# Performance work log

Measured on AMD Instinct MI355X. Metric: run time of the kernel, lower is better.

The kernel has to match this reference:

```python
import jax, jax.numpy as jnp
import numpy as np

N, E, F_IN, H, HEADS, L, DEPTH = 10000, 160000, 128, 64, 8, 6, 3
M = HEADS * H  # 512, fractal transform width
OUT_DIM = 64
EPS = 1e-5
CHAOS = 0.1


def _ln(x, g, b):
    mu = x.mean(-1, keepdims=True)
    var = x.var(-1, keepdims=True)
    return (x - mu) / jnp.sqrt(var + EPS) * g + b


def _ln_plain(x):
    mu = x.mean(-1, keepdims=True)
    var = x.var(-1, keepdims=True)
    return (x - mu) / jnp.sqrt(var + EPS)


def setup_inputs() -> dict:
    key = jax.random.key(0)
    ks = iter(jax.random.split(key, 64))
    r = lambda *s: jax.random.normal(next(ks), s, jnp.float32) * 0.05
    return dict(
        x=jax.random.normal(next(ks), (N, F_IN), jnp.float32),
        edge_index=jax.random.randint(next(ks), (2, E), 0, N),
        enc_W=r(F_IN, H), enc_b=jnp.zeros((H,)), enc_g=jnp.ones((H,)), enc_beta=jnp.zeros((H,)),
        chaos_memory=r(1, H),
        tW0=r(L, H, M), tb0=jnp.zeros((L, M)), tg0=jnp.ones((L, M)), tbeta0=jnp.zeros((L, M)),
        tW1=r(L, M, M), tb1=jnp.zeros((L, M)), tg1=jnp.ones((L, M)), tbeta1=jnp.zeros((L, M)),
        tW2=r(L, M, M), tb2=jnp.zeros((L, M)), tg2=jnp.ones((L, M)), tbeta2=jnp.zeros((L, M)),
        att=r(L, HEADS, 2 * H),
        evo_W1=r(H, 2 * H), evo_b1=jnp.zeros((2 * H,)),
        evo_W2=r(2 * H, H), evo_b2=jnp.zeros((H,)),
        dec_state_W=r(H, 1), dec_state_b=jnp.zeros((1,)),
        dec_imp_W=r(H, 1), dec_imp_b=jnp.zeros((1,)),
        dec_chaos_W=r(H, 1), dec_chaos_b=jnp.zeros((1,)),
        dec_evo_W=r(H, OUT_DIM), dec_evo_b=jnp.zeros((OUT_DIM,)),
    )


def reference(x, edge_index, enc_W, enc_b, enc_g, enc_beta, chaos_memory,
              tW0, tb0, tg0, tbeta0, tW1, tb1, tg1, tbeta1, tW2, tb2, tg2, tbeta2,
              att, evo_W1, evo_b1, evo_W2, evo_b2,
              dec_state_W, dec_state_b, dec_imp_W, dec_imp_b,
              dec_chaos_W, dec_chaos_b, dec_evo_W, dec_evo_b):
    src, dst = edge_index[0], edge_index[1]  # j -> i, aggregate at dst
    nkey = jax.random.key(42)

    # encoder (dropout inactive in eval)
    h = jax.nn.relu(_ln(x @ enc_W + enc_b, enc_g, enc_beta))
    h = h + chaos_memory * CHAOS  # [1,H] broadcast

    residuals = []
    for i in range(L):
        cf = CHAOS * (1.0 + 0.1 * i)
        h_prev = h
        # fractal transform stack: pre-noise features are averaged
        Ws = [(tW0[i], tb0[i], tg0[i], tbeta0[i]),
              (tW1[i], tb1[i], tg1[i], tbeta1[i]),
              (tW2[i], tb2[i], tg2[i], tbeta2[i])]
        cur = h
        feats = 0.0
        for d, (W, b, g, be) in enumerate(Ws):
            cur = jax.nn.relu(_ln(cur @ W + b, g, be))
            feats = feats + cur
            noise = jax.random.normal(jax.random.fold_in(nkey, i * 10 + d), cur.shape, cur.dtype)
            cur = cur + noise * cf  # chaotic perturbation feeds next depth only
        hm = (feats / DEPTH).reshape(-1, HEADS, H)  # [N, heads, out]
        # GAT-style edge attention: alpha_e = <[x_i||x_j], att>
        a_i = jnp.einsum('nhc,hc->nh', hm, att[i][:, :H])
        a_j = jnp.einsum('nhc,hc->nh', hm, att[i][:, H:])
        alpha = jax.nn.leaky_relu(a_i[dst] + a_j[src], 0.2)  # [E, heads]
        # segment softmax over incoming edges of each dst node
        amax = jax.ops.segment_max(alpha, dst, num_segments=N)
        ex = jnp.exp(alpha - amax[dst])
        denom = jax.ops.segment_sum(ex, dst, num_segments=N)
        w = ex / denom[dst]  # [E, heads]
        msg = hm[src] * w[:, :, None]  # [E, heads, out]
        agg = jax.ops.segment_sum(msg, dst, num_segments=N)  # [N, heads, out]
        h_new = agg.mean(axis=1)  # head-mean -> [N, H]
        gate = jax.nn.sigmoid(jnp.tanh(jax.nn.relu(h_new @ evo_W1 + evo_b1) @ evo_W2 + evo_b2))
        h = gate * h_new + (1.0 - gate) * h_prev
        residuals.append(h)
        h = _ln_plain(h)  # F.layer_norm without affine
    h_multi = sum(residuals) / L
    # batch is None -> decoders applied per-node on h_multi
    state = h_multi @ dec_state_W + dec_state_b
    importance = h_multi @ dec_imp_W + dec_imp_b
    chaos = h_multi @ dec_chaos_W + dec_chaos_b
    evolution = h_multi @ dec_evo_W + dec_evo_b
    return state, importance, chaos, evolution, h_multi
```

## Files before the change

### kernel.cpp

```cpp
#include <hip/hip_runtime.h>
#include <cstdint>
#include <cstddef>

#define NN 10000
#define EE 160000
#define F_IN 128
#define HH 64
#define HEADS 8
#define LL 6
#define MM 512
#define OUT_DIM 64
#define EPSF 1e-5f

typedef unsigned short ushort;
typedef __attribute__((ext_vector_type(8))) short bf16x8;
typedef __attribute__((ext_vector_type(8))) unsigned short ushort8;
typedef __attribute__((ext_vector_type(4))) float f32x4;

union U8 { ushort8 u; bf16x8 b; };

struct U2 { uint32_t a, b; };

__host__ __device__ constexpr uint32_t rotl32(uint32_t x, uint32_t d) {
  return (x << d) | (x >> (32u - d));
}

__host__ __device__ constexpr U2 threefry2x32(uint32_t k1, uint32_t k2, uint32_t x0, uint32_t x1) {
  uint32_t ks2 = k1 ^ k2 ^ 0x1BD11BDAu;
  x0 += k1; x1 += k2;
  x0 += x1; x1 = rotl32(x1, 13); x1 ^= x0;
  x0 += x1; x1 = rotl32(x1, 15); x1 ^= x0;
  x0 += x1; x1 = rotl32(x1, 26); x1 ^= x0;
  x0 += x1; x1 = rotl32(x1, 6);  x1 ^= x0;
  x0 += k2; x1 += ks2 + 1u;
  x0 += x1; x1 = rotl32(x1, 17); x1 ^= x0;
  x0 += x1; x1 = rotl32(x1, 29); x1 ^= x0;
  x0 += x1; x1 = rotl32(x1, 16); x1 ^= x0;
  x0 += x1; x1 = rotl32(x1, 24); x1 ^= x0;
  x0 += ks2; x1 += k1 + 2u;
  x0 += x1; x1 = rotl32(x1, 13); x1 ^= x0;
  x0 += x1; x1 = rotl32(x1, 15); x1 ^= x0;
  x0 += x1; x1 = rotl32(x1, 26); x1 ^= x0;
  x0 += x1; x1 = rotl32(x1, 6);  x1 ^= x0;
  x0 += k1; x1 += k2 + 3u;
  x0 += x1; x1 = rotl32(x1, 17); x1 ^= x0;
  x0 += x1; x1 = rotl32(x1, 29); x1 ^= x0;
  x0 += x1; x1 = rotl32(x1, 16); x1 ^= x0;
  x0 += x1; x1 = rotl32(x1, 24); x1 ^= x0;
  x0 += k2; x1 += ks2 + 4u;
  x0 += x1; x1 = rotl32(x1, 13); x1 ^= x0;
  x0 += x1; x1 = rotl32(x1, 15); x1 ^= x0;
  x0 += x1; x1 = rotl32(x1, 26); x1 ^= x0;
  x0 += x1; x1 = rotl32(x1, 6);  x1 ^= x0;
  x0 += ks2; x1 += k1 + 5u;
  return U2{x0, x1};
}

__host__ __device__ constexpr U2 foldKey(uint32_t data) {
  return threefry2x32(0u, 42u, 0u, data);
}

__device__ inline float erfinv_f32(float x) {
  float w = -log1pf(-x * x);
  float p;
  if (w < 5.0f) {
    w -= 2.5f;
    p = 2.81022636e-08f;
    p = fmaf(p, w, 3.43273939e-07f);
    p = fmaf(p, w, -3.5233877e-06f);
    p = fmaf(p, w, -4.39150654e-06f);
    p = fmaf(p, w, 0.00021858087f);
    p = fmaf(p, w, -0.00125372503f);
    p = fmaf(p, w, -0.00417768164f);
    p = fmaf(p, w, 0.246640727f);
    p = fmaf(p, w, 1.50140941f);
  } else {
    w = sqrtf(w) - 3.0f;
    p = -0.000200214257f;
    p = fmaf(p, w, 0.000100950558f);
    p = fmaf(p, w, 0.00134934322f);
    p = fmaf(p, w, -0.00367342844f);
    p = fmaf(p, w, 0.00573950773f);
    p = fmaf(p, w, -0.0076224613f);
    p = fmaf(p, w, 0.00943887047f);
    p = fmaf(p, w, 1.00167406f);
    p = fmaf(p, w, 2.83297682f);
  }
  return p * x;
}

__device__ inline float jax_normal(uint32_t k1, uint32_t k2, uint32_t idx) {
  U2 r = threefry2x32(k1, k2, 0u, idx);
  uint32_t bits = r.a ^ r.b;
  uint32_t fb = (bits >> 9) | 0x3f800000u;
  float f = __uint_as_float(fb) - 1.0f;
  const float lo = -0.99999994f;
  float u = f * 2.0f + lo;
  u = fmaxf(lo, u);
  return 1.41421356f * erfinv_f32(u);
}

__device__ inline float waveSum(float v) {
  v += __shfl_xor(v, 32, 64);
  v += __shfl_xor(v, 16, 64);
  v += __shfl_xor(v, 8, 64);
  v += __shfl_xor(v, 4, 64);
  v += __shfl_xor(v, 2, 64);
  v += __shfl_xor(v, 1, 64);
  return v;
}

__device__ inline ushort bf16rn(float x) {
  uint32_t u = __float_as_uint(x);
  uint32_t r = (u + 0x7fffu + ((u >> 16) & 1u)) >> 16;
  return (ushort)r;
}
__device__ inline float bf16tof(ushort h) {
  return __uint_as_float(((uint32_t)h) << 16);
}


__global__ __launch_bounds__(64) void encoder_kernel(
    const float* __restrict__ x, const float* __restrict__ W, const float* __restrict__ b,
    const float* __restrict__ g, const float* __restrict__ be, const float* __restrict__ cm,
    float* __restrict__ h, ushort* __restrict__ hHi, ushort* __restrict__ hLo) {
  __shared__ float xs[F_IN];
  int n = blockIdx.x, l = threadIdx.x;
  xs[l]      = x[(size_t)n * F_IN + l];
  xs[l + 64] = x[(size_t)n * F_IN + 64 + l];
  __syncthreads();
  float acc = b[l];
  #pragma unroll 8
  for (int k = 0; k < F_IN; k++) acc = fmaf(xs[k], W[k * HH + l], acc);
  float mu = waveSum(acc) * (1.0f / 64.0f);
  float d = acc - mu;
  float var = waveSum(d * d) * (1.0f / 64.0f);
  float y = fmaf(d / sqrtf(var + EPSF), g[l], be[l]);
  y = fmaxf(y, 0.0f);
  float hv = fmaf(cm[l], 0.1f, y);
  h[(size_t)n * HH + l] = hv;
  ushort hi = bf16rn(hv);
  size_t oi = ((size_t)(l >> 5) * NN + n) * 32 + (l & 31);
  hHi[oi] = hi;
  hLo[oi] = bf16rn(hv - bf16tof(hi));
}

__global__ __launch_bounds__(256) void wconv(
    const float* __restrict__ W, ushort* __restrict__ oh, ushort* __restrict__ ol, int K) {
  __shared__ ushort Th[64][40], Tl[64][40];
  int kt = blockIdx.x;
  int m0 = blockIdx.y * 64;
  int lay = blockIdx.z;
  const float* Wl = W + (size_t)lay * K * MM;
  ushort* ohl = oh + (size_t)lay * K * MM;
  ushort* oll = ol + (size_t)lay * K * MM;
  int t = threadIdx.x;
  #pragma unroll
  for (int p = 0; p < 2; ++p) {
    int li = p * 256 + t;
    int k = li >> 4, mg = (li & 15) * 4;
    float4 v = *(const float4*)(Wl + (size_t)(kt * 32 + k) * MM + m0 + mg);
    float vv[4] = {v.x, v.y, v.z, v.w};
    #pragma unroll
    for (int q = 0; q < 4; ++q) {
      ushort hi = bf16rn(vv[q]);
      Th[mg + q][k] = hi;
      Tl[mg + q][k] = bf16rn(vv[q] - bf16tof(hi));
    }
  }
  __syncthreads();
  #pragma unroll
  for (int p = 0; p < 2; ++p) {
    int li = p * 256 + t;
    int plane = li >> 8;
    int rem = li & 255;
    int m = rem >> 2, kh = (rem & 3) * 8;
    size_t go = ((size_t)kt * MM + m0 + m) * 32 + kh;
    if (plane == 0) *(ushort8*)(ohl + go) = *(const ushort8*)&Th[m][kh];
    else            *(ushort8*)(oll + go) = *(const ushort8*)&Tl[m][kh];
  }
}

__global__ __launch_bounds__(256) void gemm_mfma(
    const ushort* __restrict__ Ahg, const ushort* __restrict__ Alg,
    const ushort* __restrict__ Whg, const ushort* __restrict__ Wlg,
    const float* __restrict__ bias, float* __restrict__ C, int nkt) {
  __shared__ __align__(16) ushort Ah[128][36], Al[128][36];
  __shared__ __align__(16) ushort Bh[64][36],  Bl[64][36];
  int t = threadIdx.x, w = t >> 6, lane = t & 63;
  int lr = lane & 15, r4 = lane >> 4, kh = r4 * 8;
  int gid = blockIdx.x;
  int xcd = gid & 7, q = gid >> 3;
  int lrow = q >> 3, colp = q & 7;
  int rowTile = xcd * 10 + lrow;
  if (rowTile >= 79) return;
  int row0 = rowTile * 128, col0 = colp * 64;
  int wr = (w & 1) * 64, wc = (w >> 1) * 32;
  f32x4 acc[4][2];
  #pragma unroll
  for (int i = 0; i < 4; i++)
    #pragma unroll
    for (int j = 0; j < 2; j++) acc[i][j] = (f32x4){0.f, 0.f, 0.f, 0.f};

  for (int kt = 0; kt < nkt; ++kt) {
    #pragma unroll
    for (int p = 0; p < 2; ++p) {
      int li = p * 256 + t;
      int r = li >> 2, kq = (li & 3) * 8;
      int n = row0 + r;
      ushort8 va = {0,0,0,0,0,0,0,0}, vl = {0,0,0,0,0,0,0,0};
      if (n < NN) {
        size_t so = ((size_t)kt * NN + n) * 32 + kq;
        va = *(const ushort8*)(Ahg + so);
        vl = *(const ushort8*)(Alg + so);
      }
      *(ushort8*)&Ah[r][kq] = va;
      *(ushort8*)&Al[r][kq] = vl;
    }
    {
      int c = t >> 2, kq = (t & 3) * 8;
      size_t so = ((size_t)kt * MM + col0 + c) * 32 + kq;
      *(ushort8*)&Bh[c][kq] = *(const ushort8*)(Whg + so);
      *(ushort8*)&Bl[c][kq] = *(const ushort8*)(Wlg + so);
    }
    __syncthreads();
    bf16x8 bh[2], bl[2];
    #pragma unroll
    for (int cf = 0; cf < 2; ++cf) {
      bh[cf] = *(const bf16x8*)&Bh[wc + cf * 16 + lr][kh];
      bl[cf] = *(const bf16x8*)&Bl[wc + cf * 16 + lr][kh];
    }
    #pragma unroll
    for (int rf = 0; rf < 4; ++rf) {
      bf16x8 ah = *(const bf16x8*)&Ah[wr + rf * 16 + lr][kh];
      bf16x8 al = *(const bf16x8*)&Al[wr + rf * 16 + lr][kh];
      #pragma unroll
      for (int cf = 0; cf < 2; ++cf) {
        acc[rf][cf] = __builtin_amdgcn_mfma_f32_16x16x32_bf16(ah, bh[cf], acc[rf][cf], 0, 0, 0);
        acc[rf][cf] = __builtin_amdgcn_mfma_f32_16x16x32_bf16(ah, bl[cf], acc[rf][cf], 0, 0, 0);
        acc[rf][cf] = __builtin_amdgcn_mfma_f32_16x16x32_bf16(al, bh[cf], acc[rf][cf], 0, 0, 0);
      }
    }
    __syncthreads();
  }
  #pragma unroll
  for (int cf = 0; cf < 2; ++cf) {
    int c = col0 + wc + cf * 16 + lr;
    float bc = bias[c];
    #pragma unroll
    for (int rf = 0; rf < 4; ++rf) {
      #pragma unroll
      for (int j = 0; j < 4; ++j) {
        int r = row0 + wr + rf * 16 + r4 * 4 + j;
        if (r < NN) C[(size_t)r * MM + c] = acc[rf][cf][j] + bc;
      }
    }
  }
}

__global__ __launch_bounds__(256) void ln_relu_acc(
    const float* __restrict__ Y, const float* __restrict__ g, const float* __restrict__ be,
    float* __restrict__ feats, int firstDepth,
    ushort* __restrict__ outHi, ushort* __restrict__ outLo,
    uint32_t k1, uint32_t k2, float cf,
    const float* __restrict__ attL, float* __restrict__ ai, float* __restrict__ aj,
    uint32_t* __restrict__ featsPk) {
  int n = blockIdx.x, t = threadIdx.x;
  size_t base = (size_t)n * MM;
  float v0 = Y[base + t], v1 = Y[base + t + 256];
  int wid = t >> 6, lane = t & 63;
  __shared__ float red[8];
  __shared__ float fsh[512];
  float s = waveSum(v0 + v1);
  if (lane == 0) red[wid] = s;
  __syncthreads();
  float mu = (red[0] + red[1] + red[2] + red[3]) * (1.0f / 512.0f);
  float d0 = v0 - mu, d1 = v1 - mu;
  float q = waveSum(d0 * d0 + d1 * d1);
  if (lane == 0) red[4 + wid] = q;
  __syncthreads();
  float var = (red[4] + red[5] + red[6] + red[7]) * (1.0f / 512.0f);
  float inv = 1.0f / sqrtf(var + EPSF);
  float o0 = fmaxf(fmaf(d0 * inv, g[t], be[t]), 0.0f);
  float o1 = fmaxf(fmaf(d1 * inv, g[t + 256], be[t + 256]), 0.0f);
  float f0, f1;
  if (firstDepth) { f0 = o0; f1 = o1; }
  else { f0 = feats[base + t] + o0; f1 = feats[base + t + 256] + o1; }
  if (outHi) {
    feats[base + t] = f0; feats[base + t + 256] = f1;
    float y0 = fmaf(jax_normal(k1, k2, (uint32_t)(base + t)), cf, o0);
    float y1 = fmaf(jax_normal(k1, k2, (uint32_t)(base + t + 256)), cf, o1);
    int c0 = t, c1 = t + 256;
    size_t i0 = ((size_t)(c0 >> 5) * NN + n) * 32 + (c0 & 31);
    size_t i1 = ((size_t)(c1 >> 5) * NN + n) * 32 + (c1 & 31);
    ushort h0 = bf16rn(y0), h1 = bf16rn(y1);
    outHi[i0] = h0; outLo[i0] = bf16rn(y0 - bf16tof(h0));
    outHi[i1] = h1; outLo[i1] = bf16rn(y1 - bf16tof(h1));
  }
  if (attL) {
    const float inv3 = 1.0f / 3.0f;
    float w0 = f0 * inv3, w1 = f1 * inv3;
    fsh[t] = w0; fsh[t + 256] = w1;
    float si0 = waveSum(w0 * attL[wid * 128 + lane]);
    float sj0 = waveSum(w0 * attL[wid * 128 + 64 + lane]);
    float si1 = waveSum(w1 * attL[(wid + 4) * 128 + lane]);
    float sj1 = waveSum(w1 * attL[(wid + 4) * 128 + 64 + lane]);
    if (lane == 0) {
      ai[n * HEADS + wid] = si0;     aj[n * HEADS + wid] = sj0;
      ai[n * HEADS + wid + 4] = si1; aj[n * HEADS + wid + 4] = sj1;
    }
    __syncthreads();
    int p = t >> 6, ch = t & 63;
    uint32_t word = (uint32_t)bf16rn(fsh[(2 * p) * 64 + ch]) |
                    ((uint32_t)bf16rn(fsh[(2 * p + 1) * 64 + ch]) << 16);
    featsPk[(size_t)n * 256 + (size_t)((p >> 1) * 128 + 2 * ch + (p & 1))] = word;
  }
}

__global__ __launch_bounds__(256) void csr_histo(const int* __restrict__ dst, int* __restrict__ deg) {
  int e = blockIdx.x * blockDim.x + threadIdx.x;
  if (e < EE) atomicAdd(&deg[dst[e]], 1);
}

__global__ __launch_bounds__(256) void csr_scan(const int* __restrict__ deg, int* __restrict__ offs) {
  __shared__ int part[256];
  int t = threadIdx.x;
  const int chunk = (NN + 255) / 256;
  int start = t * chunk;
  int s = 0;
  for (int j = 0; j < chunk; j++) { int i = start + j; if (i < NN) s += deg[i]; }
  part[t] = s; __syncthreads();
  for (int d = 1; d < 256; d <<= 1) {
    int v = (t >= d) ? part[t - d] : 0;
    __syncthreads();
    part[t] += v;
    __syncthreads();
  }
  int run = (t == 0) ? 0 : part[t - 1];
  for (int j = 0; j < chunk; j++) {
    int i = start + j;
    if (i < NN) { offs[i] = run; run += deg[i]; }
  }
  if (t == 0) offs[NN] = EE;
}

__global__ __launch_bounds__(256) void csr_fill(const int* __restrict__ src, const int* __restrict__ dst,
                                                int* __restrict__ pos, int* __restrict__ csrc) {
  int e = blockIdx.x * blockDim.x + threadIdx.x;
  if (e >= EE) return;
  int d = dst[e];
  int slot = atomicAdd(&pos[d], 1);
  csrc[slot] = src[e];
}

__global__ __launch_bounds__(256) void gat_fused(
    const int* __restrict__ offs, const int* __restrict__ csrc,
    const float* __restrict__ ai, const float* __restrict__ aj,
    const uint32_t* __restrict__ featsPk,
    const float* __restrict__ W1, const float* __restrict__ b1,
    const float* __restrict__ W2, const float* __restrict__ b2,
    float* __restrict__ h, float* __restrict__ resid,
    ushort* __restrict__ hHi, ushort* __restrict__ hLo) {
  int n = blockIdx.x, t = threadIdx.x, wid = t >> 6, l = t & 63;
  int pair = wid >> 1, hpg = wid & 1, hBase = hpg * 4;
  int e0 = offs[n], e1 = offs[n + 1];
  float aiv[4];
  *(float4*)aiv = *(const float4*)&ai[(size_t)n * 8 + hBase];
  float m[4];
  #pragma unroll
  for (int q = 0; q < 4; ++q) m[q] = aiv[q] + 4.0f;

  __shared__ int sSrc[64];
  __shared__ float sEx[8][64];
  __shared__ float denSh[8];
  float acc[4] = {0.f, 0.f, 0.f, 0.f};
  float den[4] = {0.f, 0.f, 0.f, 0.f};

  for (int c = e0; c < e1; c += 64) {
    int idx = c + l;
    bool act = idx < e1;
    if (wid < 2) {
      float ex[4] = {0.f, 0.f, 0.f, 0.f};
      if (act) {
        int sv = csrc[idx];
        if (wid == 0) sSrc[l] = sv;
        float ajv[4];
        *(float4*)ajv = *(const float4*)&aj[(size_t)sv * 8 + hBase];
        #pragma unroll
        for (int q = 0; q < 4; ++q) {
          float a = aiv[q] + ajv[q];
          a = (a >= 0.f) ? a : 0.2f * a;
          ex[q] = expf(a - m[q]);
          den[q] += ex[q];
        }
      }
      #pragma unroll
      for (int q = 0; q < 4; ++q) sEx[hBase + q][l] = ex[q];
    }
    __syncthreads();
    int cnt = min(64, e1 - c);
    int j = pair;
    for (; j + 6 < cnt; j += 8) {
      const uint32_t* b0 = featsPk + (size_t)sSrc[j]     * 256;
      const uint32_t* b1p = featsPk + (size_t)sSrc[j + 2] * 256;
      const uint32_t* b2p = featsPk + (size_t)sSrc[j + 4] * 256;
      const uint32_t* b3 = featsPk + (size_t)sSrc[j + 6] * 256;
      uint2 v0 = *((const uint2*)b0 + hpg * 64 + l);
      uint2 v1 = *((const uint2*)b1p + hpg * 64 + l);
      uint2 v2 = *((const uint2*)b2p + hpg * 64 + l);
      uint2 v3 = *((const uint2*)b3 + hpg * 64 + l);
      acc[0] = fmaf(bf16tof((ushort)(v0.x & 0xffffu)), sEx[hBase + 0][j], acc[0]);
      acc[1] = fmaf(bf16tof((ushort)(v0.x >> 16)),     sEx[hBase + 1][j], acc[1]);
      acc[2] = fmaf(bf16tof((ushort)(v0.y & 0xffffu)), sEx[hBase + 2][j], acc[2]);
      acc[3] = fmaf(bf16tof((ushort)(v0.y >> 16)),     sEx[hBase + 3][j], acc[3]);
      acc[0] = fmaf(bf16tof((ushort)(v1.x & 0xffffu)), sEx[hBase + 0][j + 2], acc[0]);
      acc[1] = fmaf(bf16tof((ushort)(v1.x >> 16)),     sEx[hBase + 1][j + 2], acc[1]);
      acc[2] = fmaf(bf16tof((ushort)(v1.y & 0xffffu)), sEx[hBase + 2][j + 2], acc[2]);
      acc[3] = fmaf(bf16tof((ushort)(v1.y >> 16)),     sEx[hBase + 3][j + 2], acc[3]);
      acc[0] = fmaf(bf16tof((ushort)(v2.x & 0xffffu)), sEx[hBase + 0][j + 4], acc[0]);
      acc[1] = fmaf(bf16tof((ushort)(v2.x >> 16)),     sEx[hBase + 1][j + 4], acc[1]);
      acc[2] = fmaf(bf16tof((ushort)(v2.y & 0xffffu)), sEx[hBase + 2][j + 4], acc[2]);
      acc[3] = fmaf(bf16tof((ushort)(v2.y >> 16)),     sEx[hBase + 3][j + 4], acc[3]);
      acc[0] = fmaf(bf16tof((ushort)(v3.x & 0xffffu)), sEx[hBase + 0][j + 6], acc[0]);
      acc[1] = fmaf(bf16tof((ushort)(v3.x >> 16)),     sEx[hBase + 1][j + 6], acc[1]);
      acc[2] = fmaf(bf16tof((ushort)(v3.y & 0xffffu)), sEx[hBase + 2][j + 6], acc[2]);
      acc[3] = fmaf(bf16tof((ushort)(v3.y >> 16)),     sEx[hBase + 3][j + 6], acc[3]);
    }
    for (; j < cnt; j += 2) {
      uint2 v = *((const uint2*)(featsPk + (size_t)sSrc[j] * 256) + hpg * 64 + l);
      acc[0] = fmaf(bf16tof((ushort)(v.x & 0xffffu)), sEx[hBase + 0][j], acc[0]);
      acc[1] = fmaf(bf16tof((ushort)(v.x >> 16)),     sEx[hBase + 1][j], acc[1]);
      acc[2] = fmaf(bf16tof((ushort)(v.y & 0xffffu)), sEx[hBase + 2][j], acc[2]);
      acc[3] = fmaf(bf16tof((ushort)(v.y >> 16)),     sEx[hBase + 3][j], acc[3]);
    }
    __syncthreads();
  }

  if (wid < 2) {
    #pragma unroll
    for (int q = 0; q < 4; ++q) den[q] = waveSum(den[q]);
    if (l == 0) {
      #pragma unroll
      for (int q = 0; q < 4; ++q) denSh[hBase + q] = den[q];
    }
  }
  __syncthreads();
  float hsum = 0.f;
  #pragma unroll
  for (int q = 0; q < 4; ++q) {
    float d = denSh[hBase + q];
    hsum += acc[q] * ((d > 0.f) ? (1.0f / d) : 0.f);
  }

  __shared__ float hacc[4][64];
  hacc[wid][l] = hsum;
  __syncthreads();
  __shared__ float hn[64];
  __shared__ float z[128];
  if (t < 64) hn[t] = (hacc[0][t] + hacc[1][t] + hacc[2][t] + hacc[3][t]) * 0.125f;
  __syncthreads();
  if (t < 128) {
    float zz = b1[t];
    #pragma unroll 8
    for (int k = 0; k < 64; k++) zz = fmaf(hn[k], W1[k * 128 + t], zz);
    z[t] = fmaxf(zz, 0.f);
  }
  __syncthreads();
  if (t < 64) {
    float y = b2[t];
    #pragma unroll 8
    for (int k = 0; k < 128; k++) y = fmaf(z[k], W2[k * 64 + t], y);
    float gate = 1.0f / (1.0f + expf(-tanhf(y)));
    float hp = h[(size_t)n * HH + t];
    float hb = gate * hn[t] + (1.0f - gate) * hp;
    resid[(size_t)n * HH + t] += hb;
    float mu = waveSum(hb) * (1.0f / 64.0f);
    float dd = hb - mu;
    float var = waveSum(dd * dd) * (1.0f / 64.0f);
    float hv = dd / sqrtf(var + EPSF);
    h[(size_t)n * HH + t] = hv;
    ushort hi = bf16rn(hv);
    size_t oi = ((size_t)(t >> 5) * NN + n) * 32 + (t & 31);
    hHi[oi] = hi;
    hLo[oi] = bf16rn(hv - bf16tof(hi));
  }
}

__global__ __launch_bounds__(64) void decoder_kernel(
    const float* __restrict__ resid,
    const float* __restrict__ dsW, const float* __restrict__ dsb,
    const float* __restrict__ diW, const float* __restrict__ dib,
    const float* __restrict__ dcW, const float* __restrict__ dcb,
    const float* __restrict__ deW, const float* __restrict__ deb,
    float* __restrict__ out) {
  __shared__ float hm[64];
  int n = blockIdx.x, l = threadIdx.x;
  float v = resid[(size_t)n * HH + l] * (1.0f / 6.0f);
  hm[l] = v;
  float s1 = waveSum(v * dsW[l]);
  float s2 = waveSum(v * diW[l]);
  float s3 = waveSum(v * dcW[l]);
  if (l == 0) {
    out[n]          = s1 + dsb[0];
    out[NN + n]     = s2 + dib[0];
    out[2 * NN + n] = s3 + dcb[0];
  }
  __syncthreads();
  float e = deb[l];
  #pragma unroll 8
  for (int k = 0; k < 64; k++) e = fmaf(hm[k], deW[k * OUT_DIM + l], e);
  out[3 * NN + (size_t)n * OUT_DIM + l] = e;
  out[3 * NN + (size_t)NN * OUT_DIM + (size_t)n * HH + l] = v;
}

extern "C" void kernel_launch(void* const* d_in, const int* in_sizes, int n_in,
                              void* d_out, int out_size, void* d_ws, size_t ws_size,
                              hipStream_t stream) {
  const float* x        = (const float*)d_in[0];
  const int*   ei       = (const int*)d_in[1];
  const float* enc_W    = (const float*)d_in[2];
  const float* enc_b    = (const float*)d_in[3];
  const float* enc_g    = (const float*)d_in[4];
  const float* enc_beta = (const float*)d_in[5];
  const float* cm       = (const float*)d_in[6];
  const float* tW0 = (const float*)d_in[7];  const float* tb0 = (const float*)d_in[8];
  const float* tg0 = (const float*)d_in[9];  const float* tbe0 = (const float*)d_in[10];
  const float* tW1 = (const float*)d_in[11]; const float* tb1 = (const float*)d_in[12];
  const float* tg1 = (const float*)d_in[13]; const float* tbe1 = (const float*)d_in[14];
  const float* tW2 = (const float*)d_in[15]; const float* tb2 = (const float*)d_in[16];
  const float* tg2 = (const float*)d_in[17]; const float* tbe2 = (const float*)d_in[18];
  const float* att = (const float*)d_in[19];
  const float* evo_W1 = (const float*)d_in[20]; const float* evo_b1 = (const float*)d_in[21];
  const float* evo_W2 = (const float*)d_in[22]; const float* evo_b2 = (const float*)d_in[23];
  const float* dsW = (const float*)d_in[24]; const float* dsb = (const float*)d_in[25];
  const float* diW = (const float*)d_in[26]; const float* dib = (const float*)d_in[27];
  const float* dcW = (const float*)d_in[28]; const float* dcb = (const float*)d_in[29];
  const float* deW = (const float*)d_in[30]; const float* deb = (const float*)d_in[31];
  float* out = (float*)d_out;

  const int* src = ei;
  const int* dst = ei + EE;

  float* ws = (float*)d_ws;
  size_t o = 0;
  float* h     = ws + o; o += (size_t)NN * HH;
  float* resid = ws + o; o += (size_t)NN * HH;
  float* ai    = ws + o; o += (size_t)NN * HEADS;
  float* aj    = ws + o; o += (size_t)NN * HEADS;
  float* Cbuf  = ws + o; o += (size_t)NN * MM;
  float* feats = ws + o; o += (size_t)NN * MM;
  int* deg  = (int*)(ws + o); o += NN;
  int* offs = (int*)(ws + o); o += NN + 2;
  int* pos  = (int*)(ws + o); o += NN;
  int* csrc = (int*)(ws + o); o += EE;
  o = (o + 3) & ~(size_t)3;
  uint32_t* featsPk = (uint32_t*)(ws + o); o += (size_t)NN * 256;
  ushort* us = (ushort*)(ws + o);
  size_t uo = 0;
  ushort* W0h = us + uo; uo += (size_t)LL * HH * MM;
  ushort* W0l = us + uo; uo += (size_t)LL * HH * MM;
  ushort* W1h = us + uo; uo += (size_t)LL * MM * MM;
  ushort* W1l = us + uo; uo += (size_t)LL * MM * MM;
  ushort* W2h = us + uo; uo += (size_t)LL * MM * MM;
  ushort* W2l = us + uo; uo += (size_t)LL * MM * MM;
  ushort* hHi = us + uo; uo += (size_t)NN * HH;
  ushort* hLo = us + uo; uo += (size_t)NN * HH;
  ushort* actHi = us + uo; uo += (size_t)NN * MM;
  ushort* actLo = us + uo; uo += (size_t)NN * MM;
  (void)ws_size; (void)n_in; (void)in_sizes; (void)out_size;

  wconv<<<dim3(2, 8, 6), 256, 0, stream>>>(tW0, W0h, W0l, HH);
  wconv<<<dim3(16, 8, 6), 256, 0, stream>>>(tW1, W1h, W1l, MM);
  wconv<<<dim3(16, 8, 6), 256, 0, stream>>>(tW2, W2h, W2l, MM);

  hipMemsetAsync(deg, 0, (size_t)NN * sizeof(int), stream);
  csr_histo<<<(EE + 255) / 256, 256, 0, stream>>>(dst, deg);
  csr_scan<<<1, 256, 0, stream>>>(deg, offs);
  hipMemcpyAsync(pos, offs, (size_t)NN * sizeof(int), hipMemcpyDeviceToDevice, stream);
  csr_fill<<<(EE + 255) / 256, 256, 0, stream>>>(src, dst, pos, csrc);

  encoder_kernel<<<NN, 64, 0, stream>>>(x, enc_W, enc_b, enc_g, enc_beta, cm, h, hHi, hLo);
  hipMemsetAsync(resid, 0, (size_t)NN * HH * sizeof(float), stream);

  const int GEMM_GRID = 640;
  for (int i = 0; i < LL; ++i) {
    float cfac = (float)(0.1 * (1.0 + 0.1 * (double)i));
    U2 fk0 = foldKey((uint32_t)(i * 10 + 0));
    U2 fk1 = foldKey((uint32_t)(i * 10 + 1));
    const float* attL = att + (size_t)i * HEADS * 2 * HH;

    gemm_mfma<<<GEMM_GRID, 256, 0, stream>>>(hHi, hLo,
        W0h + (size_t)i * HH * MM, W0l + (size_t)i * HH * MM, tb0 + (size_t)i * MM, Cbuf, 2);
    ln_relu_acc<<<NN, 256, 0, stream>>>(Cbuf, tg0 + (size_t)i * MM, tbe0 + (size_t)i * MM,
        feats, 1, actHi, actLo, fk0.a, fk0.b, cfac, nullptr, nullptr, nullptr, nullptr);

    gemm_mfma<<<GEMM_GRID, 256, 0, stream>>>(actHi, actLo,
        W1h + (size_t)i * MM * MM, W1l + (size_t)i * MM * MM, tb1 + (size_t)i * MM, Cbuf, 16);
    ln_relu_acc<<<NN, 256, 0, stream>>>(Cbuf, tg1 + (size_t)i * MM, tbe1 + (size_t)i * MM,
        feats, 0, actHi, actLo, fk1.a, fk1.b, cfac, nullptr, nullptr, nullptr, nullptr);

    gemm_mfma<<<GEMM_GRID, 256, 0, stream>>>(actHi, actLo,
        W2h + (size_t)i * MM * MM, W2l + (size_t)i * MM * MM, tb2 + (size_t)i * MM, Cbuf, 16);
    ln_relu_acc<<<NN, 256, 0, stream>>>(Cbuf, tg2 + (size_t)i * MM, tbe2 + (size_t)i * MM,
        feats, 0, nullptr, nullptr, 0u, 0u, 0.f, attL, ai, aj, featsPk);

    gat_fused<<<NN, 256, 0, stream>>>(offs, csrc, ai, aj, featsPk,
        evo_W1, evo_b1, evo_W2, evo_b2, h, resid, hHi, hLo);
  }

  decoder_kernel<<<NN, 64, 0, stream>>>(resid, dsW, dsb, diW, dib, dcW, dcb, deW, deb, out);
}
```

Before: 1.364 ms.

## Store GEMM output as bf16 and remap GAT aggregation to one wave per node

The GEMM epilogue now writes its pre-LayerNorm output as bf16 instead of fp32, and ln_relu_acc reads bf16. This halves the traffic of the intermediate buffer but adds rounding error before the LayerNorm. Separately, gat_fused is rewritten so each 64-lane wave handles one destination node, with all 8 heads, 16-byte feature loads and no block-level syncs. The gate MLP now also runs inside that wave. This removes the __syncthreads overhead and the idle waves of the previous one-block-per-node layout.

```diff
diff --git a/kernel.cpp b/kernel.cpp
--- a/kernel.cpp
+++ b/kernel.cpp
@@ -184,7 +184,7 @@
 __global__ __launch_bounds__(256) void gemm_mfma(
     const ushort* __restrict__ Ahg, const ushort* __restrict__ Alg,
     const ushort* __restrict__ Whg, const ushort* __restrict__ Wlg,
-    const float* __restrict__ bias, float* __restrict__ C, int nkt) {
+    const float* __restrict__ bias, ushort* __restrict__ C, int nkt) {
   __shared__ __align__(16) ushort Ah[128][36], Al[128][36];
   __shared__ __align__(16) ushort Bh[64][36],  Bl[64][36];
   int t = threadIdx.x, w = t >> 6, lane = t & 63;
@@ -252,14 +252,14 @@
       #pragma unroll
       for (int j = 0; j < 4; ++j) {
         int r = row0 + wr + rf * 16 + r4 * 4 + j;
-        if (r < NN) C[(size_t)r * MM + c] = acc[rf][cf][j] + bc;
+        if (r < NN) C[(size_t)r * MM + c] = bf16rn(acc[rf][cf][j] + bc);
       }
     }
   }
 }
 
 __global__ __launch_bounds__(256) void ln_relu_acc(
-    const float* __restrict__ Y, const float* __restrict__ g, const float* __restrict__ be,
+    const ushort* __restrict__ Y, const float* __restrict__ g, const float* __restrict__ be,
     float* __restrict__ feats, int firstDepth,
     ushort* __restrict__ outHi, ushort* __restrict__ outLo,
     uint32_t k1, uint32_t k2, float cf,
@@ -267,7 +267,7 @@
     uint32_t* __restrict__ featsPk) {
   int n = blockIdx.x, t = threadIdx.x;
   size_t base = (size_t)n * MM;
-  float v0 = Y[base + t], v1 = Y[base + t + 256];
+  float v0 = bf16tof(Y[base + t]), v1 = bf16tof(Y[base + t + 256]);
   int wid = t >> 6, lane = t & 63;
   __shared__ float red[8];
   __shared__ float fsh[512];
@@ -361,129 +361,99 @@
     const float* __restrict__ W2, const float* __restrict__ b2,
     float* __restrict__ h, float* __restrict__ resid,
     ushort* __restrict__ hHi, ushort* __restrict__ hLo) {
-  int n = blockIdx.x, t = threadIdx.x, wid = t >> 6, l = t & 63;
-  int pair = wid >> 1, hpg = wid & 1, hBase = hpg * 4;
+  __shared__ int   sSrc[4][64];
+  __shared__ float sEx[4][8][64];
+  __shared__ float hnSh[4][64];
+  __shared__ float zSh[4][128];
+  int t = threadIdx.x, wid = t >> 6, l = t & 63;
+  int n = blockIdx.x * 4 + wid;
   int e0 = offs[n], e1 = offs[n + 1];
-  float aiv[4];
-  *(float4*)aiv = *(const float4*)&ai[(size_t)n * 8 + hBase];
-  float m[4];
+  int ph = l >> 5;
+  float aiv[8];
+  *(float4*)&aiv[0] = *(const float4*)&ai[(size_t)n * 8];
+  *(float4*)&aiv[4] = *(const float4*)&ai[(size_t)n * 8 + 4];
+  float m[8];
   #pragma unroll
-  for (int q = 0; q < 4; ++q) m[q] = aiv[q] + 4.0f;
-
-  __shared__ int sSrc[64];
-  __shared__ float sEx[8][64];
-  __shared__ float denSh[8];
-  float acc[4] = {0.f, 0.f, 0.f, 0.f};
-  float den[4] = {0.f, 0.f, 0.f, 0.f};
+  for (int q = 0; q < 8; ++q) m[q] = aiv[q] + 4.0f;
+
+  float exAcc[8] = {0.f, 0.f, 0.f, 0.f, 0.f, 0.f, 0.f, 0.f};
+  float acc[8]   = {0.f, 0.f, 0.f, 0.f, 0.f, 0.f, 0.f, 0.f};
 
   for (int c = e0; c < e1; c += 64) {
-    int idx = c + l;
-    bool act = idx < e1;
-    if (wid < 2) {
-      float ex[4] = {0.f, 0.f, 0.f, 0.f};
-      if (act) {
-        int sv = csrc[idx];
-        if (wid == 0) sSrc[l] = sv;
-        float ajv[4];
-        *(float4*)ajv = *(const float4*)&aj[(size_t)sv * 8 + hBase];
-        #pragma unroll
-        for (int q = 0; q < 4; ++q) {
-          float a = aiv[q] + ajv[q];
-          a = (a >= 0.f) ? a : 0.2f * a;
-          ex[q] = expf(a - m[q]);
-          den[q] += ex[q];
-        }
+    int cnt = min(64, e1 - c);
+    if (l < cnt) {
+      int sv = csrc[c + l];
+      sSrc[wid][l] = sv;
+      float ajv[8];
+      *(float4*)&ajv[0] = *(const float4*)&aj[(size_t)sv * 8];
+      *(float4*)&ajv[4] = *(const float4*)&aj[(size_t)sv * 8 + 4];
+      #pragma unroll
+      for (int q = 0; q < 8; ++q) {
+        float a = aiv[q] + ajv[q];
+        a = (a >= 0.f) ? a : 0.2f * a;
+        float ex = expf(a - m[q]);
+        sEx[wid][q][l] = ex;
+        exAcc[q] += ex;
       }
-      #pragma unroll
-      for (int q = 0; q < 4; ++q) sEx[hBase + q][l] = ex[q];
-    }
-    __syncthreads();
-    int cnt = min(64, e1 - c);
-    int j = pair;
-    for (; j + 6 < cnt; j += 8) {
-      const uint32_t* b0 = featsPk + (size_t)sSrc[j]     * 256;
-      const uint32_t* b1p = featsPk + (size_t)sSrc[j + 2] * 256;
-      const uint32_t* b2p = featsPk + (size_t)sSrc[j + 4] * 256;
-      const uint32_t* b3 = featsPk + (size_t)sSrc[j + 6] * 256;
-      uint2 v0 = *((const uint2*)b0 + hpg * 64 + l);
-      uint2 v1 = *((const uint2*)b1p + hpg * 64 + l);
-      uint2 v2 = *((const uint2*)b2p + hpg * 64 + l);
-      uint2 v3 = *((const uint2*)b3 + hpg * 64 + l);
-      acc[0] = fmaf(bf16tof((ushort)(v0.x & 0xffffu)), sEx[hBase + 0][j], acc[0]);
-      acc[1] = fmaf(bf16tof((ushort)(v0.x >> 16)),     sEx[hBase + 1][j], acc[1]);
-      acc[2] = fmaf(bf16tof((ushort)(v0.y & 0xffffu)), sEx[hBase + 2][j], acc[2]);
-      acc[3] = fmaf(bf16tof((ushort)(v0.y >> 16)),     sEx[hBase + 3][j], acc[3]);
-      acc[0] = fmaf(bf16tof((ushort)(v1.x & 0xffffu)), sEx[hBase + 0][j + 2], acc[0]);
-      acc[1] = fmaf(bf16tof((ushort)(v1.x >> 16)),     sEx[hBase + 1][j + 2], acc[1]);
-      acc[2] = fmaf(bf16tof((ushort)(v1.y & 0xffffu)), sEx[hBase + 2][j + 2], acc[2]);
-      acc[3] = fmaf(bf16tof((ushort)(v1.y >> 16)),     sEx[hBase + 3][j + 2], acc[3]);
-      acc[0] = fmaf(bf16tof((ushort)(v2.x & 0xffffu)), sEx[hBase + 0][j + 4], acc[0]);
-      acc[1] = fmaf(bf16tof((ushort)(v2.x >> 16)),     sEx[hBase + 1][j + 4], acc[1]);
-      acc[2] = fmaf(bf16tof((ushort)(v2.y & 0xffffu)), sEx[hBase + 2][j + 4], acc[2]);
-      acc[3] = fmaf(bf16tof((ushort)(v2.y >> 16)),     sEx[hBase + 3][j + 4], acc[3]);
-      acc[0] = fmaf(bf16tof((ushort)(v3.x & 0xffffu)), sEx[hBase + 0][j + 6], acc[0]);
-      acc[1] = fmaf(bf16tof((ushort)(v3.x >> 16)),     sEx[hBase + 1][j + 6], acc[1]);
-      acc[2] = fmaf(bf16tof((ushort)(v3.y & 0xffffu)), sEx[hBase + 2][j + 6], acc[2]);
-      acc[3] = fmaf(bf16tof((ushort)(v3.y >> 16)),     sEx[hBase + 3][j + 6], acc[3]);
-    }
-    for (; j < cnt; j += 2) {
-      uint2 v = *((const uint2*)(featsPk + (size_t)sSrc[j] * 256) + hpg * 64 + l);
-      acc[0] = fmaf(bf16tof((ushort)(v.x & 0xffffu)), sEx[hBase + 0][j], acc[0]);
-      acc[1] = fmaf(bf16tof((ushort)(v.x >> 16)),     sEx[hBase + 1][j], acc[1]);
-      acc[2] = fmaf(bf16tof((ushort)(v.y & 0xffffu)), sEx[hBase + 2][j], acc[2]);
-      acc[3] = fmaf(bf16tof((ushort)(v.y >> 16)),     sEx[hBase + 3][j], acc[3]);
-    }
-    __syncthreads();
-  }
-
-  if (wid < 2) {
-    #pragma unroll
-    for (int q = 0; q < 4; ++q) den[q] = waveSum(den[q]);
-    if (l == 0) {
-      #pragma unroll
-      for (int q = 0; q < 4; ++q) denSh[hBase + q] = den[q];
-    }
-  }
-  __syncthreads();
-  float hsum = 0.f;
+    }
+    #pragma unroll 2
+    for (int j = 0; j < cnt; ++j) {
+      int sv = sSrc[wid][j];
+      uint4 v = *(const uint4*)(featsPk + (size_t)sv * 256 + l * 4);
+      float w0 = sEx[wid][4 * ph + 0][j];
+      float w1v = sEx[wid][4 * ph + 1][j];
+      float w2v = sEx[wid][4 * ph + 2][j];
+      float w3v = sEx[wid][4 * ph + 3][j];
+      acc[0] = fmaf(bf16tof((ushort)(v.x & 0xffffu)), w0,  acc[0]);
+      acc[1] = fmaf(bf16tof((ushort)(v.x >> 16)),     w1v, acc[1]);
+      acc[2] = fmaf(bf16tof((ushort)(v.y & 0xffffu)), w2v, acc[2]);
+      acc[3] = fmaf(bf16tof((ushort)(v.y >> 16)),     w3v, acc[3]);
+      acc[4] = fmaf(bf16tof((ushort)(v.z & 0xffffu)), w0,  acc[4]);
+      acc[5] = fmaf(bf16tof((ushort)(v.z >> 16)),     w1v, acc[5]);
+      acc[6] = fmaf(bf16tof((ushort)(v.w & 0xffffu)), w2v, acc[6]);
+      acc[7] = fmaf(bf16tof((ushort)(v.w >> 16)),     w3v, acc[7]);
+    }
+  }
+  float id[8];
   #pragma unroll
-  for (int q = 0; q < 4; ++q) {
-    float d = denSh[hBase + q];
-    hsum += acc[q] * ((d > 0.f) ? (1.0f / d) : 0.f);
-  }
-
-  __shared__ float hacc[4][64];
-  hacc[wid][l] = hsum;
-  __syncthreads();
-  __shared__ float hn[64];
-  __shared__ float z[128];
-  if (t < 64) hn[t] = (hacc[0][t] + hacc[1][t] + hacc[2][t] + hacc[3][t]) * 0.125f;
-  __syncthreads();
-  if (t < 128) {
-    float zz = b1[t];
-    #pragma unroll 8
-    for (int k = 0; k < 64; k++) zz = fmaf(hn[k], W1[k * 128 + t], zz);
-    z[t] = fmaxf(zz, 0.f);
-  }
-  __syncthreads();
-  if (t < 64) {
-    float y = b2[t];
-    #pragma unroll 8
-    for (int k = 0; k < 128; k++) y = fmaf(z[k], W2[k * 64 + t], y);
-    float gate = 1.0f / (1.0f + expf(-tanhf(y)));
-    float hp = h[(size_t)n * HH + t];
-    float hb = gate * hn[t] + (1.0f - gate) * hp;
-    resid[(size_t)n * HH + t] += hb;
-    float mu = waveSum(hb) * (1.0f / 64.0f);
-    float dd = hb - mu;
-    float var = waveSum(dd * dd) * (1.0f / 64.0f);
-    float hv = dd / sqrtf(var + EPSF);
-    h[(size_t)n * HH + t] = hv;
-    ushort hi = bf16rn(hv);
-    size_t oi = ((size_t)(t >> 5) * NN + n) * 32 + (t & 31);
-    hHi[oi] = hi;
-    hLo[oi] = bf16rn(hv - bf16tof(hi));
-  }
+  for (int q = 0; q < 8; ++q) {
+    float d = waveSum(exAcc[q]);
+    id[q] = (d > 0.f) ? (1.0f / d) : 0.f;
+  }
+  float s0 = acc[0] * id[4 * ph + 0] + acc[1] * id[4 * ph + 1]
+           + acc[2] * id[4 * ph + 2] + acc[3] * id[4 * ph + 3];
+  float s1 = acc[4] * id[4 * ph + 0] + acc[5] * id[4 * ph + 1]
+           + acc[6] * id[4 * ph + 2] + acc[7] * id[4 * ph + 3];
+  s0 += __shfl_xor(s0, 32, 64);
+  s1 += __shfl_xor(s1, 32, 64);
+  int chB = 2 * (l & 31);
+  hnSh[wid][chB]     = s0 * 0.125f;
+  hnSh[wid][chB + 1] = s1 * 0.125f;
+  float zz0 = b1[l], zz1 = b1[l + 64];
+  #pragma unroll 8
+  for (int k = 0; k < 64; k++) {
+    float hv = hnSh[wid][k];
+    zz0 = fmaf(hv, W1[k * 128 + l], zz0);
+    zz1 = fmaf(hv, W1[k * 128 + 64 + l], zz1);
+  }
+  zSh[wid][l] = fmaxf(zz0, 0.f);
+  zSh[wid][l + 64] = fmaxf(zz1, 0.f);
+  float y = b2[l];
+  #pragma unroll 8
+  for (int k = 0; k < 128; k++) y = fmaf(zSh[wid][k], W2[k * 64 + l], y);
+  float gate = 1.0f / (1.0f + expf(-tanhf(y)));
+  float hp = h[(size_t)n * HH + l];
+  float hb = gate * hnSh[wid][l] + (1.0f - gate) * hp;
+  resid[(size_t)n * HH + l] += hb;
+  float mu = waveSum(hb) * (1.0f / 64.0f);
+  float dd = hb - mu;
+  float var = waveSum(dd * dd) * (1.0f / 64.0f);
+  float hv = dd / sqrtf(var + EPSF);
+  h[(size_t)n * HH + l] = hv;
+  ushort hi = bf16rn(hv);
+  size_t oi = ((size_t)(l >> 5) * NN + n) * 32 + (l & 31);
+  hHi[oi] = hi;
+  hLo[oi] = bf16rn(hv - bf16tof(hi));
 }
 
 __global__ __launch_bounds__(64) void decoder_kernel(
@@ -547,7 +517,6 @@
   float* resid = ws + o; o += (size_t)NN * HH;
   float* ai    = ws + o; o += (size_t)NN * HEADS;
   float* aj    = ws + o; o += (size_t)NN * HEADS;
-  float* Cbuf  = ws + o; o += (size_t)NN * MM;
   float* feats = ws + o; o += (size_t)NN * MM;
   int* deg  = (int*)(ws + o); o += NN;
   int* offs = (int*)(ws + o); o += NN + 2;
@@ -567,6 +536,7 @@
   ushort* hLo = us + uo; uo += (size_t)NN * HH;
   ushort* actHi = us + uo; uo += (size_t)NN * MM;
   ushort* actLo = us + uo; uo += (size_t)NN * MM;
+  ushort* Cbuf  = us + uo; uo += (size_t)NN * MM;
   (void)ws_size; (void)n_in; (void)in_sizes; (void)out_size;
 
   wconv<<<dim3(2, 8, 6), 256, 0, stream>>>(tW0, W0h, W0l, HH);
@@ -604,7 +574,7 @@
     ln_relu_acc<<<NN, 256, 0, stream>>>(Cbuf, tg2 + (size_t)i * MM, tbe2 + (size_t)i * MM,
         feats, 0, nullptr, nullptr, 0u, 0u, 0.f, attL, ai, aj, featsPk);
 
-    gat_fused<<<NN, 256, 0, stream>>>(offs, csrc, ai, aj, featsPk,
+    gat_fused<<<NN / 4, 256, 0, stream>>>(offs, csrc, ai, aj, featsPk,
         evo_W1, evo_b1, evo_W2, evo_b2, h, resid, hHi, hLo);
   }
 
```

New measurement: 1.303 ms. -4.5%, faster.
